# Performance work log

Measured on AMD Instinct MI355X. Metric: run time of the kernel, lower is better.

The kernel has to match this reference:

```python
import jax, jax.numpy as jnp
import numpy as np

B, S, HID = 2, 2048, 4096
NH, NKV, HD = 32, 8, 128
N_REP = NH // NKV
SCALING = HD ** -0.5


def rotate_half(x):
    x1, x2 = x[..., : x.shape[-1] // 2], x[..., x.shape[-1] // 2 :]
    return jnp.concatenate((-x2, x1), axis=-1)


def setup_inputs() -> dict:
    key = jax.random.key(0)
    ks = jax.random.split(key, 8)
    hidden_states = jax.random.normal(ks[0], (B, S, HID), dtype=jnp.float32)
    # rotary embeddings (realistic cos/sin from inverse-frequency angles)
    inv_freq = 1.0 / (10000.0 ** (jnp.arange(0, HD, 2, dtype=jnp.float32) / HD))
    pos = jnp.arange(S, dtype=jnp.float32)
    ang = pos[:, None] * inv_freq[None, :]  # [S, HD/2]
    emb = jnp.concatenate([ang, ang], axis=-1)  # [S, HD]
    cos = jnp.broadcast_to(jnp.cos(emb)[None], (B, S, HD))
    sin = jnp.broadcast_to(jnp.sin(emb)[None], (B, S, HD))
    # additive causal mask [B,1,S,S]
    causal = jnp.triu(jnp.full((S, S), -1e9, dtype=jnp.float32), k=1)
    attention_mask = jnp.broadcast_to(causal[None, None], (B, 1, S, S))
    std = HID ** -0.5
    Wq = jax.random.normal(ks[1], (NH * HD, HID), dtype=jnp.float32) * std
    Wk = jax.random.normal(ks[2], (NKV * HD, HID), dtype=jnp.float32) * std
    Wv = jax.random.normal(ks[3], (NKV * HD, HID), dtype=jnp.float32) * std
    Wo = jax.random.normal(ks[4], (HID, NH * HD), dtype=jnp.float32) * std
    return {"hidden_states": hidden_states, "cos": cos, "sin": sin,
            "attention_mask": attention_mask, "Wq": Wq, "Wk": Wk, "Wv": Wv, "Wo": Wo}


def reference(hidden_states, cos, sin, attention_mask, Wq, Wk, Wv, Wo):
    b, s, _ = hidden_states.shape
    # projections (nn.Linear: x @ W.T), reshape to [B, H, S, D]
    q = (hidden_states @ Wq.T).reshape(b, s, NH, HD).transpose(0, 2, 1, 3)
    k = (hidden_states @ Wk.T).reshape(b, s, NKV, HD).transpose(0, 2, 1, 3)
    v = (hidden_states @ Wv.T).reshape(b, s, NKV, HD).transpose(0, 2, 1, 3)
    # RoPE, cos/sin broadcast over head dim
    c, sn = cos[:, None], sin[:, None]  # [B,1,S,D]
    q = q * c + rotate_half(q) * sn
    k = k * c + rotate_half(k) * sn
    # GQA repeat_kv
    k = jnp.repeat(k, N_REP, axis=1)
    v = jnp.repeat(v, N_REP, axis=1)
    # eager attention
    attn = jnp.einsum("bhqd,bhkd->bhqk", q, k) * SCALING
    attn = attn + attention_mask[:, :, :, : k.shape[2]]
    attn = jax.nn.softmax(attn.astype(jnp.float32), axis=-1).astype(q.dtype)
    out = jnp.einsum("bhqk,bhkd->bhqd", attn, v)
    out = out.transpose(0, 2, 1, 3).reshape(b, s, NH * HD)
    return out @ Wo.T
```

## Files before the change

kernel.cpp:

```cpp
#include <hip/hip_runtime.h>


typedef __bf16 bf16x8 __attribute__((ext_vector_type(8)));
typedef __bf16 bf16x4 __attribute__((ext_vector_type(4)));
typedef float floatx4 __attribute__((ext_vector_type(4)));

#define S_LEN 2048
#define HIDN  4096
#define NH    32
#define NKV   8
#define HD    128

__device__ inline void async_copy16(const void* g, void* l) {
  __builtin_amdgcn_global_load_lds(
      (const __attribute__((address_space(1))) void*)g,
      (__attribute__((address_space(3))) void*)l, 16, 0, 0);
}

template<int N> __device__ __forceinline__ void waitv() {
  static_assert(N == 0 || N == 6, "vmcnt");
  if constexpr (N == 0) asm volatile("s_waitcnt vmcnt(0)" ::: "memory");
  else                  asm volatile("s_waitcnt vmcnt(6)" ::: "memory");
}

__global__ __launch_bounds__(256) void cvt_bf16(const float* __restrict__ src,
                                                __bf16* __restrict__ dst, int n8)
{
  int i = blockIdx.x * 256 + threadIdx.x;
  if (i >= n8) return;
  const float4* s = (const float4*)src + (size_t)i * 2;
  float4 a = s[0], b = s[1];
  bf16x8 r = {(__bf16)a.x, (__bf16)a.y, (__bf16)a.z, (__bf16)a.w,
              (__bf16)b.x, (__bf16)b.y, (__bf16)b.z, (__bf16)b.w};
  *((bf16x8*)dst + i) = r;
}

__device__ __forceinline__ void gemm_core64(
    const __bf16* __restrict__ A, const __bf16* __restrict__ WB,
    __bf16* lds, int m0, int n0, int tid, floatx4 (&acc)[4][4])
{
  constexpr int A_BYTES = 128 * 64 * 2;
  constexpr int STAGE_B = (128 + 256) * 64 * 2;
  constexpr int NK      = HIDN / 64;

  const int wave = tid >> 6, lane = tid & 63;
  const int quad = lane >> 4, l16 = lane & 15;
  const int wm = wave >> 2, wn = wave & 3;

  size_t a_src[2], b_src[4];
  #pragma unroll
  for (int ra = 0; ra < 2; ra++) {
    int idx = ra * 512 + tid;
    int row = idx >> 3, chunk = (idx & 7) ^ (row & 7);
    a_src[ra] = (size_t)(m0 + row) * HIDN + chunk * 8;
  }
  #pragma unroll
  for (int rb = 0; rb < 4; rb++) {
    int idx = rb * 512 + tid;
    int row = idx >> 3, chunk = (idx & 7) ^ (row & 7);
    b_src[rb] = (size_t)(n0 + row) * HIDN + chunk * 8;
  }

  const int swq  = (quad ^ (l16 & 3)) * 16;
  const int kxor = ((l16 >> 2) & 1) * 64;
  const int a_rd = (wm * 64 + l16) * 128 + swq;
  const int b_rd = A_BYTES + (wn * 64 + l16) * 128 + swq;

  #pragma unroll
  for (int mi = 0; mi < 4; mi++)
    #pragma unroll
    for (int ni = 0; ni < 4; ni++) acc[mi][ni] = (floatx4){0.f, 0.f, 0.f, 0.f};

  char* ldsb = (char*)lds;
  auto stage = [&](int kt, int slotB) {
    char* sb = ldsb + slotB;
    const size_t ko = (size_t)kt * 64;
    #pragma unroll
    for (int ra = 0; ra < 2; ra++)
      async_copy16(A + ko + a_src[ra], sb + (ra * 512 + tid) * 16);
    #pragma unroll
    for (int rb = 0; rb < 4; rb++)
      async_copy16(WB + ko + b_src[rb], sb + A_BYTES + (rb * 512 + tid) * 16);
  };

  stage(0, 0);
  stage(1, STAGE_B);

  int sco = 0, spo = 2 * STAGE_B;
  for (int kt = 0; kt < NK; kt++) {
    if (kt < NK - 1) waitv<6>();
    else             waitv<0>();
    __builtin_amdgcn_s_barrier();
    asm volatile("" ::: "memory");
    if (kt + 2 < NK) stage(kt + 2, spo);

    const char* sb = ldsb + sco;
    bf16x8 av[4][2], bv[4][2];
    #pragma unroll
    for (int kk = 0; kk < 2; kk++) {
      const int kb = (kk << 6) ^ kxor;
      #pragma unroll
      for (int ni = 0; ni < 4; ni++)
        bv[ni][kk] = *(const bf16x8*)(sb + b_rd + ni * 2048 + kb);
      #pragma unroll
      for (int mi = 0; mi < 4; mi++)
        av[mi][kk] = *(const bf16x8*)(sb + a_rd + mi * 2048 + kb);
    }
    __builtin_amdgcn_s_setprio(1);
    #pragma unroll
    for (int kk = 0; kk < 2; kk++)
      #pragma unroll
      for (int mi = 0; mi < 4; mi++)
        #pragma unroll
        for (int ni = 0; ni < 4; ni++)
          acc[mi][ni] = __builtin_amdgcn_mfma_f32_16x16x32_bf16(
              bv[ni][kk], av[mi][kk], acc[mi][ni], 0, 0, 0);
    __builtin_amdgcn_s_setprio(0);

    sco += STAGE_B; if (sco == 3 * STAGE_B) sco = 0;
    spo += STAGE_B; if (spo == 3 * STAGE_B) spo = 0;
  }
}

__global__ __launch_bounds__(512, 2) void qkv_gemm_bf16(
    const __bf16* __restrict__ A, const __bf16* __restrict__ WB,
    __bf16* __restrict__ Qb, __bf16* __restrict__ Kb, __bf16* __restrict__ Vt)
{
  __shared__ __bf16 lds[3 * (128 + 256) * 32 * 2];
  const int tid = threadIdx.x;
  const int m0 = blockIdx.y * 128, n0 = blockIdx.x * 256;
  floatx4 acc[4][4];
  gemm_core64(A, WB, lds, m0, n0, tid, acc);

  const int wave = tid >> 6, lane = tid & 63;
  const int quad = lane >> 4, l16 = lane & 15;
  const int wm = wave >> 2, wn = wave & 3;
  #pragma unroll
  for (int mi = 0; mi < 4; mi++) {
    int m = m0 + wm * 64 + mi * 16 + l16;
    int b = m >> 11, s = m & (S_LEN - 1);
    #pragma unroll
    for (int ni = 0; ni < 4; ni++) {
      int nb = n0 + wn * 64 + ni * 16 + quad * 4;
      if (nb < 4096) {
        int hh = nb >> 7, d = nb & 127;
        bf16x4 v = {(__bf16)acc[mi][ni][0], (__bf16)acc[mi][ni][1],
                    (__bf16)acc[mi][ni][2], (__bf16)acc[mi][ni][3]};
        *(bf16x4*)&Qb[(((size_t)b * NH + hh) * S_LEN + s) * HD + d] = v;
      } else if (nb < 5120) {
        int nl = nb - 4096, hh = nl >> 7, d = nl & 127;
        bf16x4 v = {(__bf16)acc[mi][ni][0], (__bf16)acc[mi][ni][1],
                    (__bf16)acc[mi][ni][2], (__bf16)acc[mi][ni][3]};
        *(bf16x4*)&Kb[(((size_t)b * NKV + hh) * S_LEN + s) * HD + d] = v;
      } else {
        int nl = nb - 5120, hh = nl >> 7, d = nl & 127;
        #pragma unroll
        for (int r = 0; r < 4; r++)
          Vt[(((size_t)b * NKV + hh) * HD + d + r) * S_LEN + s] =
              (__bf16)acc[mi][ni][r];
      }
    }
  }
}

__global__ __launch_bounds__(512, 2) void out_gemm_bf16(
    const __bf16* __restrict__ A, const __bf16* __restrict__ WB,
    float* __restrict__ C)
{
  __shared__ __bf16 lds[3 * (128 + 256) * 32 * 2];
  const int tid = threadIdx.x;
  const int m0 = blockIdx.y * 128, n0 = blockIdx.x * 256;
  floatx4 acc[4][4];
  gemm_core64(A, WB, lds, m0, n0, tid, acc);

  const int wave = tid >> 6, lane = tid & 63;
  const int quad = lane >> 4, l16 = lane & 15;
  const int wm = wave >> 2, wn = wave & 3;
  #pragma unroll
  for (int mi = 0; mi < 4; mi++) {
    int m = m0 + wm * 64 + mi * 16 + l16;
    #pragma unroll
    for (int ni = 0; ni < 4; ni++) {
      int nb = n0 + wn * 64 + ni * 16 + quad * 4;
      *(floatx4*)&C[(size_t)m * HIDN + nb] = acc[mi][ni];
    }
  }
}

__global__ __launch_bounds__(256) void qkv_gemm_f32(
    const float* __restrict__ A, const float* __restrict__ Wq,
    const float* __restrict__ Wk, const float* __restrict__ Wv,
    __bf16* __restrict__ Qb, __bf16* __restrict__ Kb, __bf16* __restrict__ Vt)
{
  __shared__ __bf16 As[128 * 40];
  __shared__ __bf16 Bs[128 * 40];
  const int tid  = threadIdx.x;
  const int wave = tid >> 6, lane = tid & 63;
  const int quad = lane >> 4, l16 = lane & 15;
  const int wrow = (wave >> 1) * 64, wcol = (wave & 1) * 64;
  const int m0 = blockIdx.y * 128;
  const int n0 = blockIdx.x * 128;

  const float* W; int wr0; int sel;
  if (n0 < 4096)      { W = Wq; wr0 = n0;        sel = 0; }
  else if (n0 < 5120) { W = Wk; wr0 = n0 - 4096; sel = 1; }
  else                { W = Wv; wr0 = n0 - 5120; sel = 2; }

  floatx4 acc[4][4];
  #pragma unroll
  for (int i = 0; i < 4; i++)
    #pragma unroll
    for (int j = 0; j < 4; j++) acc[i][j] = (floatx4){0.f, 0.f, 0.f, 0.f};

  for (int k0 = 0; k0 < HIDN; k0 += 32) {
    __syncthreads();
    #pragma unroll
    for (int it = 0; it < 4; ++it) {
      int c = tid + it * 256;
      int row = c >> 3, c4 = (c & 7) * 4;
      float4 va = *(const float4*)(A + (size_t)(m0 + row) * HIDN + k0 + c4);
      __bf16* da = &As[row * 40 + c4];
      da[0] = (__bf16)va.x; da[1] = (__bf16)va.y; da[2] = (__bf16)va.z; da[3] = (__bf16)va.w;
      float4 vb = *(const float4*)(W + (size_t)(wr0 + row) * HIDN + k0 + c4);
      __bf16* db = &Bs[row * 40 + c4];
      db[0] = (__bf16)vb.x; db[1] = (__bf16)vb.y; db[2] = (__bf16)vb.z; db[3] = (__bf16)vb.w;
    }
    __syncthreads();
    bf16x8 af[4], bfr[4];
    #pragma unroll
    for (int i = 0; i < 4; i++)
      af[i] = *(const bf16x8*)&As[(wrow + i * 16 + l16) * 40 + quad * 8];
    #pragma unroll
    for (int j = 0; j < 4; j++)
      bfr[j] = *(const bf16x8*)&Bs[(wcol + j * 16 + l16) * 40 + quad * 8];
    #pragma unroll
    for (int i = 0; i < 4; i++)
      #pragma unroll
      for (int j = 0; j < 4; j++)
        acc[i][j] = __builtin_amdgcn_mfma_f32_16x16x32_bf16(af[i], bfr[j], acc[i][j], 0, 0, 0);
  }

  #pragma unroll
  for (int i = 0; i < 4; i++) {
    #pragma unroll
    for (int j = 0; j < 4; j++) {
      #pragma unroll
      for (int r = 0; r < 4; r++) {
        int m = m0 + wrow + i * 16 + quad * 4 + r;
        int n = n0 + wcol + j * 16 + l16;
        __bf16 v = (__bf16)acc[i][j][r];
        int b = m >> 11, s = m & (S_LEN - 1);
        if (sel == 0) {
          int h = n >> 7, d = n & 127;
          Qb[(((size_t)b * NH + h) * S_LEN + s) * HD + d] = v;
        } else if (sel == 1) {
          int nl = n - 4096, h = nl >> 7, d = nl & 127;
          Kb[(((size_t)b * NKV + h) * S_LEN + s) * HD + d] = v;
        } else {
          int nl = n - 5120, h = nl >> 7, d = nl & 127;
          Vt[(((size_t)b * NKV + h) * HD + d) * S_LEN + s] = v;
        }
      }
    }
  }
}

__global__ __launch_bounds__(256) void out_gemm_f32(
    const __bf16* __restrict__ A, const float* __restrict__ Wo,
    float* __restrict__ C)
{
  __shared__ __bf16 As[128 * 40];
  __shared__ __bf16 Bs[128 * 40];
  const int tid  = threadIdx.x;
  const int wave = tid >> 6, lane = tid & 63;
  const int quad = lane >> 4, l16 = lane & 15;
  const int wrow = (wave >> 1) * 64, wcol = (wave & 1) * 64;
  const int m0 = blockIdx.y * 128;
  const int n0 = blockIdx.x * 128;

  floatx4 acc[4][4];
  #pragma unroll
  for (int i = 0; i < 4; i++)
    #pragma unroll
    for (int j = 0; j < 4; j++) acc[i][j] = (floatx4){0.f, 0.f, 0.f, 0.f};

  for (int k0 = 0; k0 < HIDN; k0 += 32) {
    __syncthreads();
    #pragma unroll
    for (int it = 0; it < 2; ++it) {
      int c = tid + it * 256;
      int row = c >> 2, c8 = (c & 3) * 8;
      *(bf16x8*)&As[row * 40 + c8] =
          *(const bf16x8*)(A + (size_t)(m0 + row) * HIDN + k0 + c8);
    }
    #pragma unroll
    for (int it = 0; it < 4; ++it) {
      int c = tid + it * 256;
      int row = c >> 3, c4 = (c & 7) * 4;
      float4 vb = *(const float4*)(Wo + (size_t)(n0 + row) * HIDN + k0 + c4);
      __bf16* db = &Bs[row * 40 + c4];
      db[0] = (__bf16)vb.x; db[1] = (__bf16)vb.y; db[2] = (__bf16)vb.z; db[3] = (__bf16)vb.w;
    }
    __syncthreads();
    bf16x8 af[4], bfr[4];
    #pragma unroll
    for (int i = 0; i < 4; i++)
      af[i] = *(const bf16x8*)&As[(wrow + i * 16 + l16) * 40 + quad * 8];
    #pragma unroll
    for (int j = 0; j < 4; j++)
      bfr[j] = *(const bf16x8*)&Bs[(wcol + j * 16 + l16) * 40 + quad * 8];
    #pragma unroll
    for (int i = 0; i < 4; i++)
      #pragma unroll
      for (int j = 0; j < 4; j++)
        acc[i][j] = __builtin_amdgcn_mfma_f32_16x16x32_bf16(af[i], bfr[j], acc[i][j], 0, 0, 0);
  }

  #pragma unroll
  for (int i = 0; i < 4; i++)
    #pragma unroll
    for (int j = 0; j < 4; j++)
      #pragma unroll
      for (int r = 0; r < 4; r++) {
        int m = m0 + wrow + i * 16 + quad * 4 + r;
        int n = n0 + wcol + j * 16 + l16;
        C[(size_t)m * HIDN + n] = acc[i][j][r];
      }
}

__global__ __launch_bounds__(256) void rope_kernel(
    __bf16* __restrict__ Qb, __bf16* __restrict__ Kb,
    const float* __restrict__ cosp, const float* __restrict__ sinp)
{
  size_t i = (size_t)blockIdx.x * 256 + threadIdx.x;
  const size_t QP = (size_t)2 * NH * S_LEN * 64;
  __bf16* buf; int H; size_t t;
  if (i < QP) { buf = Qb; H = NH;  t = i; }
  else        { buf = Kb; H = NKV; t = i - QP; }
  int d = (int)(t & 63);
  int s = (int)((t >> 6) & (S_LEN - 1));
  size_t rest = t >> 17;
  int h = (int)(rest % H);
  int b = (int)(rest / H);
  size_t base = (((size_t)b * H + h) * S_LEN + s) * HD;
  float q0 = (float)buf[base + d];
  float q1 = (float)buf[base + d + 64];
  float c  = cosp[((size_t)b * S_LEN + s) * HD + d];
  float sn = sinp[((size_t)b * S_LEN + s) * HD + d];
  buf[base + d]      = (__bf16)(q0 * c - q1 * sn);
  buf[base + d + 64] = (__bf16)(q1 * c + q0 * sn);
}

__global__ __launch_bounds__(256, 2) void flash_attn(
    const __bf16* __restrict__ Q, const __bf16* __restrict__ Kc,
    const __bf16* __restrict__ Vt, __bf16* __restrict__ Out)
{
  __shared__ __bf16 Ks[64 * 136];
  __shared__ __bf16 VTs[128 * 72];
  __shared__ __bf16 Ps[4 * 32 * 72];
  const int tid  = threadIdx.x;
  const int wave = tid >> 6, lane = tid & 63;
  const int quad = lane >> 4, l16 = lane & 15;
  const int bh = blockIdx.x;
  const int h = bh & 31, b = bh >> 5;
  const int qt = 15 - (int)blockIdx.y;
  const int kvh = h >> 2;
  const size_t qbase  = (((size_t)b * NH + h) * S_LEN + qt * 128 + wave * 32) * HD;
  const size_t kbase  = ((size_t)b * NKV + kvh) * S_LEN * HD;
  const size_t vtbase = ((size_t)b * NKV + kvh) * (size_t)HD * S_LEN;
  const int psbase = wave * (32 * 72);

  bf16x8 qf[2][4];
  #pragma unroll
  for (int st = 0; st < 2; st++)
    #pragma unroll
    for (int kk = 0; kk < 4; kk++)
      qf[st][kk] = *(const bf16x8*)&Q[qbase + (size_t)(st * 16 + l16) * HD + kk * 32 + quad * 8];

  floatx4 o[2][8];
  floatx4 ol[2];
  #pragma unroll
  for (int st = 0; st < 2; st++) {
    ol[st] = (floatx4){0.f, 0.f, 0.f, 0.f};
    #pragma unroll
    for (int ct = 0; ct < 8; ct++) o[st][ct] = (floatx4){0.f, 0.f, 0.f, 0.f};
  }
  bf16x8 onesv;
  #pragma unroll
  for (int u = 0; u < 8; u++) onesv[u] = (__bf16)1.0f;

  const float c1 = 0.12753785f;
  const float c2 = -28.853900f;
  const int kj_end = 2 * qt + 2;

  bf16x8 kreg[4], vreg[4];
  #pragma unroll
  for (int it = 0; it < 4; ++it) {
    int c = tid + it * 256;
    kreg[it] = *(const bf16x8*)&Kc[kbase + (size_t)((c >> 4)) * HD + (c & 15) * 8];
    vreg[it] = *(const bf16x8*)&Vt[vtbase + (size_t)(c >> 3) * S_LEN + (c & 7) * 8];
  }

  for (int kj = 0; kj < kj_end; ++kj) {
    __syncthreads();
    #pragma unroll
    for (int it = 0; it < 4; ++it) {
      int c = tid + it * 256;
      *(bf16x8*)&Ks[(c >> 4) * 136 + (c & 15) * 8] = kreg[it];
      *(bf16x8*)&VTs[(c >> 3) * 72 + (c & 7) * 8] = vreg[it];
    }
    __syncthreads();

    if (kj + 1 < kj_end) {
      #pragma unroll
      for (int it = 0; it < 4; ++it) {
        int c = tid + it * 256;
        kreg[it] = *(const bf16x8*)&Kc[kbase + (size_t)((kj + 1) * 64 + (c >> 4)) * HD + (c & 15) * 8];
        vreg[it] = *(const bf16x8*)&Vt[vtbase + (size_t)(c >> 3) * S_LEN + (kj + 1) * 64 + (c & 7) * 8];
      }
    }

    floatx4 s[2][4];
    #pragma unroll
    for (int st = 0; st < 2; st++)
      #pragma unroll
      for (int j = 0; j < 4; j++) s[st][j] = (floatx4){0.f, 0.f, 0.f, 0.f};
    #pragma unroll
    for (int kk = 0; kk < 4; kk++) {
      bf16x8 ak[4];
      #pragma unroll
      for (int j = 0; j < 4; j++)
        ak[j] = *(const bf16x8*)&Ks[(j * 16 + l16) * 136 + kk * 32 + quad * 8];
      __builtin_amdgcn_s_setprio(1);
      #pragma unroll
      for (int st = 0; st < 2; st++)
        #pragma unroll
        for (int j = 0; j < 4; j++)
          s[st][j] = __builtin_amdgcn_mfma_f32_16x16x32_bf16(ak[j], qf[st][kk], s[st][j], 0, 0, 0);
      __builtin_amdgcn_s_setprio(0);
    }

    #pragma unroll
    for (int st = 0; st < 2; st++) {
      const int qrow = qt * 128 + wave * 32 + st * 16 + l16;
      #pragma unroll
      for (int j = 0; j < 4; j++) {
        const int kvb = kj * 64 + j * 16 + quad * 4;
        bf16x4 pw;
        #pragma unroll
        for (int r = 0; r < 4; r++) {
          float p = __builtin_amdgcn_exp2f(fmaf(s[st][j][r], c1, c2));
          if (kvb + r > qrow) p = 0.0f;
          pw[r] = (__bf16)p;
        }
        *(bf16x4*)&Ps[psbase + (st * 16 + l16) * 72 + j * 16 + quad * 4] = pw;
      }
    }

    #pragma unroll
    for (int kk = 0; kk < 2; kk++) {
      bf16x8 bv[8];
      #pragma unroll
      for (int ct = 0; ct < 8; ct++)
        bv[ct] = *(const bf16x8*)&VTs[(ct * 16 + l16) * 72 + kk * 32 + quad * 8];
      bf16x8 ap[2];
      #pragma unroll
      for (int st = 0; st < 2; st++)
        ap[st] = *(const bf16x8*)&Ps[psbase + (st * 16 + l16) * 72 + kk * 32 + quad * 8];
      __builtin_amdgcn_s_setprio(1);
      #pragma unroll
      for (int st = 0; st < 2; st++) {
        ol[st] = __builtin_amdgcn_mfma_f32_16x16x32_bf16(ap[st], onesv, ol[st], 0, 0, 0);
        #pragma unroll
        for (int ct = 0; ct < 8; ct++)
          o[st][ct] = __builtin_amdgcn_mfma_f32_16x16x32_bf16(ap[st], bv[ct], o[st][ct], 0, 0, 0);
      }
      __builtin_amdgcn_s_setprio(0);
    }
  }

  #pragma unroll
  for (int st = 0; st < 2; st++) {
    #pragma unroll
    for (int r = 0; r < 4; r++) {
      float rl = 1.0f / ol[st][r];
      int qi = qt * 128 + wave * 32 + st * 16 + quad * 4 + r;
      #pragma unroll
      for (int ct = 0; ct < 8; ct++) {
        Out[((size_t)b * S_LEN + qi) * HIDN + h * HD + ct * 16 + l16] =
            (__bf16)(o[st][ct][r] * rl);
      }
    }
  }
}

extern "C" void kernel_launch(void* const* d_in, const int* in_sizes, int n_in,
                              void* d_out, int out_size, void* d_ws, size_t ws_size,
                              hipStream_t stream)
{
  const float* hs   = (const float*)d_in[0];
  const float* cosp = (const float*)d_in[1];
  const float* sinp = (const float*)d_in[2];
  const float* Wq   = (const float*)d_in[4];
  const float* Wk   = (const float*)d_in[5];
  const float* Wv   = (const float*)d_in[6];
  const float* Wo   = (const float*)d_in[7];
  float* out = (float*)d_out;

  __bf16* Qb  = (__bf16*)d_ws;
  __bf16* Kb  = Qb  + (size_t)16777216;
  __bf16* Vtb = Kb  + (size_t)4194304;

  if (ws_size >= (size_t)134217728) {
    __bf16* HSB = Vtb + (size_t)4194304;
    __bf16* AO  = HSB;
    __bf16* WB  = HSB + (size_t)16777216;

    cvt_bf16<<<8192, 256, 0, stream>>>(hs, HSB, 2097152);
    cvt_bf16<<<8192, 256, 0, stream>>>(Wq, WB, 2097152);
    cvt_bf16<<<2048, 256, 0, stream>>>(Wk, WB + 16777216, 524288);
    cvt_bf16<<<2048, 256, 0, stream>>>(Wv, WB + 20971520, 524288);
    qkv_gemm_bf16<<<dim3(24, 32), 512, 0, stream>>>(HSB, WB, Qb, Kb, Vtb);
    cvt_bf16<<<8192, 256, 0, stream>>>(Wo, WB, 2097152);
    rope_kernel<<<40960, 256, 0, stream>>>(Qb, Kb, cosp, sinp);
    flash_attn<<<dim3(64, 16), 256, 0, stream>>>(Qb, Kb, Vtb, AO);
    out_gemm_bf16<<<dim3(16, 32), 512, 0, stream>>>(AO, WB, out);
  } else {
    __bf16* AO = Vtb + (size_t)4194304;
    qkv_gemm_f32<<<dim3(48, 32), 256, 0, stream>>>(hs, Wq, Wk, Wv, Qb, Kb, Vtb);
    rope_kernel<<<40960, 256, 0, stream>>>(Qb, Kb, cosp, sinp);
    flash_attn<<<dim3(64, 16), 256, 0, stream>>>(Qb, Kb, Vtb, AO);
    out_gemm_f32<<<dim3(32, 32), 256, 0, stream>>>(AO, Wo, out);
  }
}
```

Baseline: 655.2 us.

## Software-pipeline LDS fragment reads in GEMM core and vectorize RoPE kernel

Restructures the bf16 GEMM main loop so that LDS fragment reads for the next k-tile are issued before the MFMAs of the current tile, using two register fragment sets and a rotating triple-buffered LDS schedule. It also switches global source offsets from size_t to int. Separately, it vectorizes the RoPE kernel so each thread handles 8 elements with 16-byte bf16 and float4 loads, cutting the launch grid by 8x. The double fragment buffers raise register pressure under 512-thread, 2-block launch bounds, and the int offsets assume products stay within 32-bit range.

Result: slower. 672.9 us (+2.7%).

```diff
diff --git a/kernel.cpp b/kernel.cpp
--- a/kernel.cpp
+++ b/kernel.cpp
@@ -41,24 +41,23 @@
 {
   constexpr int A_BYTES = 128 * 64 * 2;
   constexpr int STAGE_B = (128 + 256) * 64 * 2;
-  constexpr int NK      = HIDN / 64;
 
   const int wave = tid >> 6, lane = tid & 63;
   const int quad = lane >> 4, l16 = lane & 15;
   const int wm = wave >> 2, wn = wave & 3;
 
-  size_t a_src[2], b_src[4];
+  int a_off[2], b_off[4];
   #pragma unroll
   for (int ra = 0; ra < 2; ra++) {
     int idx = ra * 512 + tid;
     int row = idx >> 3, chunk = (idx & 7) ^ (row & 7);
-    a_src[ra] = (size_t)(m0 + row) * HIDN + chunk * 8;
+    a_off[ra] = (m0 + row) * HIDN + chunk * 8;
   }
   #pragma unroll
   for (int rb = 0; rb < 4; rb++) {
     int idx = rb * 512 + tid;
     int row = idx >> 3, chunk = (idx & 7) ^ (row & 7);
-    b_src[rb] = (size_t)(n0 + row) * HIDN + chunk * 8;
+    b_off[rb] = (n0 + row) * HIDN + chunk * 8;
   }
 
   const int swq  = (quad ^ (l16 & 3)) * 16;
@@ -77,25 +76,13 @@
     const size_t ko = (size_t)kt * 64;
     #pragma unroll
     for (int ra = 0; ra < 2; ra++)
-      async_copy16(A + ko + a_src[ra], sb + (ra * 512 + tid) * 16);
+      async_copy16(A + ko + a_off[ra], sb + (ra * 512 + tid) * 16);
     #pragma unroll
     for (int rb = 0; rb < 4; rb++)
-      async_copy16(WB + ko + b_src[rb], sb + A_BYTES + (rb * 512 + tid) * 16);
+      async_copy16(WB + ko + b_off[rb], sb + A_BYTES + (rb * 512 + tid) * 16);
   };
-
-  stage(0, 0);
-  stage(1, STAGE_B);
-
-  int sco = 0, spo = 2 * STAGE_B;
-  for (int kt = 0; kt < NK; kt++) {
-    if (kt < NK - 1) waitv<6>();
-    else             waitv<0>();
-    __builtin_amdgcn_s_barrier();
-    asm volatile("" ::: "memory");
-    if (kt + 2 < NK) stage(kt + 2, spo);
-
-    const char* sb = ldsb + sco;
-    bf16x8 av[4][2], bv[4][2];
+  auto read_frags = [&](int slotB, bf16x8 (&av)[4][2], bf16x8 (&bv)[4][2]) {
+    const char* sb = ldsb + slotB;
     #pragma unroll
     for (int kk = 0; kk < 2; kk++) {
       const int kb = (kk << 6) ^ kxor;
@@ -106,6 +93,8 @@
       for (int mi = 0; mi < 4; mi++)
         av[mi][kk] = *(const bf16x8*)(sb + a_rd + mi * 2048 + kb);
     }
+  };
+  auto mfma_tile = [&](bf16x8 (&av)[4][2], bf16x8 (&bv)[4][2]) {
     __builtin_amdgcn_s_setprio(1);
     #pragma unroll
     for (int kk = 0; kk < 2; kk++)
@@ -116,10 +105,45 @@
           acc[mi][ni] = __builtin_amdgcn_mfma_f32_16x16x32_bf16(
               bv[ni][kk], av[mi][kk], acc[mi][ni], 0, 0, 0);
     __builtin_amdgcn_s_setprio(0);
-
-    sco += STAGE_B; if (sco == 3 * STAGE_B) sco = 0;
-    spo += STAGE_B; if (spo == 3 * STAGE_B) spo = 0;
-  }
+  };
+
+  bf16x8 avA[4][2], bvA[4][2], avB[4][2], bvB[4][2];
+
+  stage(0, 0);
+  stage(1, STAGE_B);
+  waitv<6>();
+  __builtin_amdgcn_s_barrier();
+  asm volatile("" ::: "memory");
+  read_frags(0, avA, bvA);
+
+  int oRead = STAGE_B, oStage = 2 * STAGE_B, oFree = 0;
+
+#define GBODY(KT, AVc, BVc, AVn, BVn)                          \
+  {                                                            \
+    stage((KT) + 2, oStage);                                   \
+    waitv<6>();                                                \
+    asm volatile("s_waitcnt lgkmcnt(0)" ::: "memory");         \
+    __builtin_amdgcn_s_barrier();                              \
+    asm volatile("" ::: "memory");                             \
+    read_frags(oRead, AVn, BVn);                               \
+    mfma_tile(AVc, BVc);                                       \
+    int t_ = oFree; oFree = oRead; oRead = oStage; oStage = t_;\
+  }
+
+  for (int kt = 0; kt < 62; kt += 2) {
+    GBODY(kt,     avA, bvA, avB, bvB);
+    GBODY(kt + 1, avB, bvB, avA, bvA);
+  }
+  {
+    waitv<0>();
+    asm volatile("s_waitcnt lgkmcnt(0)" ::: "memory");
+    __builtin_amdgcn_s_barrier();
+    asm volatile("" ::: "memory");
+    read_frags(oRead, avB, bvB);
+    mfma_tile(avA, bvA);
+  }
+  mfma_tile(avB, bvB);
+#undef GBODY
 }
 
 __global__ __launch_bounds__(512, 2) void qkv_gemm_bf16(
@@ -333,22 +357,35 @@
     const float* __restrict__ cosp, const float* __restrict__ sinp)
 {
   size_t i = (size_t)blockIdx.x * 256 + threadIdx.x;
-  const size_t QP = (size_t)2 * NH * S_LEN * 64;
+  const size_t QP = (size_t)2 * NH * S_LEN * 8;
   __bf16* buf; int H; size_t t;
   if (i < QP) { buf = Qb; H = NH;  t = i; }
   else        { buf = Kb; H = NKV; t = i - QP; }
-  int d = (int)(t & 63);
-  int s = (int)((t >> 6) & (S_LEN - 1));
-  size_t rest = t >> 17;
+  int d0 = (int)(t & 7) * 8;
+  int s  = (int)((t >> 3) & (S_LEN - 1));
+  size_t rest = t >> 14;
   int h = (int)(rest % H);
   int b = (int)(rest / H);
   size_t base = (((size_t)b * H + h) * S_LEN + s) * HD;
-  float q0 = (float)buf[base + d];
-  float q1 = (float)buf[base + d + 64];
-  float c  = cosp[((size_t)b * S_LEN + s) * HD + d];
-  float sn = sinp[((size_t)b * S_LEN + s) * HD + d];
-  buf[base + d]      = (__bf16)(q0 * c - q1 * sn);
-  buf[base + d + 64] = (__bf16)(q1 * c + q0 * sn);
+  bf16x8 q0 = *(const bf16x8*)&buf[base + d0];
+  bf16x8 q1 = *(const bf16x8*)&buf[base + d0 + 64];
+  size_t cbase = ((size_t)b * S_LEN + s) * HD + d0;
+  float4 c0 = *(const float4*)&cosp[cbase];
+  float4 c1 = *(const float4*)&cosp[cbase + 4];
+  float4 s0 = *(const float4*)&sinp[cbase];
+  float4 s1 = *(const float4*)&sinp[cbase + 4];
+  float cc[8] = {c0.x, c0.y, c0.z, c0.w, c1.x, c1.y, c1.z, c1.w};
+  float ss[8] = {s0.x, s0.y, s0.z, s0.w, s1.x, s1.y, s1.z, s1.w};
+  bf16x8 r0, r1;
+  #pragma unroll
+  for (int u = 0; u < 8; u++) {
+    float a  = (float)q0[u];
+    float bq = (float)q1[u];
+    r0[u] = (__bf16)(a * cc[u] - bq * ss[u]);
+    r1[u] = (__bf16)(bq * cc[u] + a * ss[u]);
+  }
+  *(bf16x8*)&buf[base + d0]      = r0;
+  *(bf16x8*)&buf[base + d0 + 64] = r1;
 }
 
 __global__ __launch_bounds__(256, 2) void flash_attn(
@@ -522,13 +559,13 @@
     cvt_bf16<<<2048, 256, 0, stream>>>(Wv, WB + 20971520, 524288);
     qkv_gemm_bf16<<<dim3(24, 32), 512, 0, stream>>>(HSB, WB, Qb, Kb, Vtb);
     cvt_bf16<<<8192, 256, 0, stream>>>(Wo, WB, 2097152);
-    rope_kernel<<<40960, 256, 0, stream>>>(Qb, Kb, cosp, sinp);
+    rope_kernel<<<5120, 256, 0, stream>>>(Qb, Kb, cosp, sinp);
     flash_attn<<<dim3(64, 16), 256, 0, stream>>>(Qb, Kb, Vtb, AO);
     out_gemm_bf16<<<dim3(16, 32), 512, 0, stream>>>(AO, WB, out);
   } else {
     __bf16* AO = Vtb + (size_t)4194304;
     qkv_gemm_f32<<<dim3(48, 32), 256, 0, stream>>>(hs, Wq, Wk, Wv, Qb, Kb, Vtb);
-    rope_kernel<<<40960, 256, 0, stream>>>(Qb, Kb, cosp, sinp);
+    rope_kernel<<<5120, 256, 0, stream>>>(Qb, Kb, cosp, sinp);
     flash_attn<<<dim3(64, 16), 256, 0, stream>>>(Qb, Kb, Vtb, AO);
     out_gemm_f32<<<dim3(32, 32), 256, 0, stream>>>(AO, Wo, out);
   }
```
